# Performance work log

Hardware: AMD Instinct MI355X
Metric: run time of the kernel (lower is better)

The kernel has to match this reference:

```python
import jax, jax.numpy as jnp
import numpy as np

N, D, H, F = 384, 512, 8, 64  # n_nodes, in/out features, heads, per-head hidden
SLOPE = 0.2


def gat_v2_layer(x, mask, W_l, W_r, a):
    """GATv2 layer (is_concat=True). x: [N, D_in]; mask: [N, N, 1] bool.

    torch semantics: g_sum[i, j] = g_l[j] + g_r[i]; e = a . LeakyReLU(g_sum);
    softmax over j (dim=1); aggregate g_r with einsum('ijh,jhf->ihf').
    attn linear nn.Linear(F, 1) is shared across heads -> a: [F].
    """
    n = x.shape[0]
    g_l = (x @ W_l).reshape(n, H, F)
    g_r = (x @ W_r).reshape(n, H, F)
    # pairwise [i, j, h, f] = g_r[i] + g_l[j]  (the big O(N^2) intermediate)
    s = jax.nn.leaky_relu(g_r[:, None] + g_l[None, :], negative_slope=SLOPE)
    e = jnp.einsum('ijhf,f->ijh', s, a)
    e = jnp.where(mask, e, -jnp.inf)
    att = jax.nn.softmax(e, axis=1)  # normalize over source nodes j
    out = jnp.einsum('ijh,jhf->ihf', att, g_r)
    return out.reshape(n, H * F)


def setup_inputs() -> dict:
    key = jax.random.key(0)
    ks = jax.random.split(key, 8)
    x = jax.random.normal(ks[0], (N, D), dtype=jnp.float32)
    adj = jax.random.randint(ks[1], (N, N, 1), 0, 2, dtype=jnp.int32)
    sd = 1.0 / np.sqrt(D)
    sa = 1.0 / np.sqrt(F)
    W_l0 = jax.random.normal(ks[2], (D, H * F), dtype=jnp.float32) * sd
    W_r0 = jax.random.normal(ks[3], (D, H * F), dtype=jnp.float32) * sd
    a0 = jax.random.normal(ks[4], (F,), dtype=jnp.float32) * sa
    W_l1 = jax.random.normal(ks[5], (H * F, H * F), dtype=jnp.float32) * sd
    W_r1 = jax.random.normal(ks[6], (H * F, H * F), dtype=jnp.float32) * sd
    a1 = jax.random.normal(ks[7], (F,), dtype=jnp.float32) * sa
    return {"x": x, "adj": adj, "W_l0": W_l0, "W_r0": W_r0, "a0": a0,
            "W_l1": W_l1, "W_r1": W_r1, "a1": a1}


def reference(x, adj, W_l0, W_r0, a0, W_l1, W_r1, a1):
    n = x.shape[0]
    # selfloop: fill diagonal of adj with 1
    idx = jnp.arange(n)
    adj = adj.at[idx, idx, 0].set(1)
    mask = adj != 0  # [N, N, 1]
    # layer 0: GATv2 -> ELU (i < n_layers-1) -> residual
    out = jax.nn.elu(gat_v2_layer(x, mask, W_l0, W_r0, a0))
    x = x + out
    # layer 1: GATv2 -> Identity -> residual
    out = gat_v2_layer(x, mask, W_l1, W_r1, a1)
    x = x + out
    return x
```

## Files before the change

### kernel.cpp

```cpp
#include <hip/hip_runtime.h>
#include <hip/hip_bf16.h>
#include <stdint.h>

typedef unsigned short ushort_t;
typedef unsigned long long u64;
typedef __attribute__((ext_vector_type(8))) short short8;
typedef __attribute__((ext_vector_type(4))) float f32x4;

#define N_NODES 384
#define HF      512

__device__ inline ushort_t f2bf(float f) {
  __hip_bfloat16 b = __float2bfloat16(f);
  return *reinterpret_cast<ushort_t*>(&b);
}
__device__ inline float bf2f_u(ushort_t u) {
  union { float f; uint32_t i; } v; v.i = ((uint32_t)u) << 16; return v.f;
}

__global__ __launch_bounds__(256) void prep(
    const float* __restrict__ x, const int* __restrict__ adj,
    const float* __restrict__ w0, const float* __restrict__ w1,
    const float* __restrict__ w2, const float* __restrict__ w3,
    ushort_t* __restrict__ WT0, ushort_t* __restrict__ WT1,
    ushort_t* __restrict__ xb, u64* __restrict__ mbits)
{
  const int z = blockIdx.z;
  const int t = threadIdx.x;
  if (z == 4) {
    int idx = (blockIdx.y * 16 + blockIdx.x) * 256 + t;
#pragma unroll
    for (int r = 0; r < 3; ++r) {
      int i = idx + r * 65536;
      xb[i] = f2bf(x[i]);
    }
    return;
  }
  if (z == 5) {
    int b = blockIdx.y * 16 + blockIdx.x;
    if (b >= 96) return;
    int wave = t >> 6, lane = t & 63;
    int row = b * 4 + wave;
#pragma unroll
    for (int w = 0; w < 6; ++w) {
      int j = w * 64 + lane;
      int v = adj[row * N_NODES + j];
      u64 m = __ballot(v != 0 || row == j);
      if (lane == 0) mbits[row * 6 + w] = m;
    }
    return;
  }
  __shared__ ushort_t tile[32][33];
  const float* W = (z == 0) ? w0 : (z == 1) ? w1 : (z == 2) ? w2 : w3;
  ushort_t* WT = ((z < 2) ? WT0 : WT1) + (z & 1) * (512 * 512);
  const int n0 = blockIdx.x * 32, k0 = blockIdx.y * 32;
#pragma unroll
  for (int qq = 0; qq < 4; ++qq) {
    int idx = t + qq * 256, r = idx >> 5, c = idx & 31;
    tile[r][c] = f2bf(W[(k0 + r) * 512 + n0 + c]);
  }
  __syncthreads();
#pragma unroll
  for (int qq = 0; qq < 4; ++qq) {
    int idx = t + qq * 256, r = idx >> 5, c = idx & 31;
    WT[(n0 + r) * 512 + k0 + c] = tile[c][r];
  }
}

__global__ __launch_bounds__(256) void gemm_mfma(
    const ushort_t* __restrict__ A, const ushort_t* __restrict__ WT,
    float* __restrict__ G, ushort_t* __restrict__ glb,
    ushort_t* __restrict__ grT)
{
  const int t = threadIdx.x;
  const int wave = t >> 6, lane = t & 63;
  const int lm = lane & 15, q = lane >> 4;
  const int m0 = blockIdx.x * 16;
  const int n0 = (blockIdx.y * 4 + wave) * 32;

  const short8* Ap = (const short8*)A;
  const short8* Bp = (const short8*)WT;
  const int arow  = (m0 + lm) * 64 + q;
  const int brow0 = (n0 + lm) * 64 + q;
  const int brow1 = (n0 + 16 + lm) * 64 + q;

  f32x4 acc0 = {0.f, 0.f, 0.f, 0.f};
  f32x4 acc1 = {0.f, 0.f, 0.f, 0.f};
#pragma unroll
  for (int kc = 0; kc < 16; ++kc) {
    short8 af = Ap[arow  + kc * 4];
    short8 b0 = Bp[brow0 + kc * 4];
    short8 b1 = Bp[brow1 + kc * 4];
    acc0 = __builtin_amdgcn_mfma_f32_16x16x32_bf16(af, b0, acc0, 0, 0, 0);
    acc1 = __builtin_amdgcn_mfma_f32_16x16x32_bf16(af, b1, acc1, 0, 0, 0);
  }
  if (n0 < 512) {
#pragma unroll
    for (int r = 0; r < 4; ++r) {
      int m = m0 + q * 4 + r;
      glb[m * HF + n0 + lm]      = f2bf(acc0[r]);
      glb[m * HF + n0 + 16 + lm] = f2bf(acc1[r]);
    }
  } else {
#pragma unroll
    for (int r = 0; r < 4; ++r) {
      int m = m0 + q * 4 + r;
      G[m * 1024 + n0 + lm]      = acc0[r];
      G[m * 1024 + n0 + 16 + lm] = acc1[r];
    }
    int c0 = n0 - 512;
    uint2 p0, p1;
    p0.x = (uint32_t)f2bf(acc0[0]) | ((uint32_t)f2bf(acc0[1]) << 16);
    p0.y = (uint32_t)f2bf(acc0[2]) | ((uint32_t)f2bf(acc0[3]) << 16);
    p1.x = (uint32_t)f2bf(acc1[0]) | ((uint32_t)f2bf(acc1[1]) << 16);
    p1.y = (uint32_t)f2bf(acc1[2]) | ((uint32_t)f2bf(acc1[3]) << 16);
    *(uint2*)&grT[(c0 + lm) * 384 + m0 + q * 4]      = p0;
    *(uint2*)&grT[(c0 + 16 + lm) * 384 + m0 + q * 4] = p1;
  }
}

template <int LAYER>
__global__ __launch_bounds__(384) void attn_fused(
    const float* __restrict__ G, const ushort_t* __restrict__ glb,
    const ushort_t* __restrict__ grT, const u64* __restrict__ mbits,
    const float* __restrict__ resid_in, const float* __restrict__ avec,
    float* __restrict__ xcur_out, ushort_t* __restrict__ x1b_out,
    float* __restrict__ f_out)
{
  __shared__ __align__(16) char smem[55296];
  ushort_t (*s_gl)[72]      = (ushort_t(*)[72])smem;
  float    (*s_e)[N_NODES]  = (float(*)[N_NODES])smem;
  ushort_t (*s_pb)[392]     = (ushort_t(*)[392])(smem + 24576);
  __shared__ float s_bri[16];
  __shared__ u64   s_mask[16][6];

  const int t = threadIdx.x;
  const int i0 = blockIdx.x * 16, h = blockIdx.y;
  const int lane = t & 63, wave = t >> 6;

  if (t >= 64 && t < 160) ((u64*)s_mask)[t - 64] = mbits[i0 * 6 + (t - 64)];
  if (t >= 128) {
    int u = t - 128, il = u >> 4, fg = u & 15;
    float4 g4 = *(const float4*)(G + (i0 + il) * 1024 + 512 + h * 64 + fg * 4);
    float4 a4 = *(const float4*)(avec + fg * 4);
    float s = a4.x * g4.x + a4.y * g4.y + a4.z * g4.z + a4.w * g4.w;
    s += __shfl_xor(s, 1); s += __shfl_xor(s, 2);
    s += __shfl_xor(s, 4); s += __shfl_xor(s, 8);
    if (fg == 0) s_bri[il] = s;
  }
#pragma unroll
  for (int rep = 0; rep < 8; ++rep) {
    int idx = rep * 384 + t, row = idx >> 3, c = idx & 7;
    *(short8*)&s_gl[row][c * 8] =
        *(const short8*)&glb[row * HF + h * 64 + c * 8];
  }
  __syncthreads();

  float gl[64];
  {
    const short8* rowp = (const short8*)&s_gl[t][0];
#pragma unroll
    for (int c = 0; c < 8; ++c) {
      short8 v = rowp[c];
#pragma unroll
      for (int u2 = 0; u2 < 8; ++u2)
        gl[c * 8 + u2] = bf2f_u((ushort_t)v[u2]);
    }
  }
  __syncthreads();

  float accl = 0.f;
#pragma unroll
  for (int f = 0; f < 64; ++f) accl += avec[f] * gl[f];

  float e_abs[16];
  for (int il = 0; il < 16; ++il) {
    const float* __restrict__ gr = G + (i0 + il) * 1024 + 512 + h * 64;
    float acc = 0.f;
#pragma unroll
    for (int f = 0; f < 64; ++f) {
      float z = gl[f] + gr[f];
      acc += avec[f] * fabsf(z);
    }
    e_abs[il] = acc;
  }
  {
    const int jw = t >> 6, jb = t & 63;
#pragma unroll
    for (int il = 0; il < 16; ++il) {
      bool m = (s_mask[il][jw] >> jb) & 1;
      float e = 0.6f * (accl + s_bri[il]) + 0.4f * e_abs[il];
      s_e[il][t] = m ? e : -1e30f;
    }
  }
  __syncthreads();

  for (int il = wave; il < 16; il += 6) {
    float v[6];
    float mx = -1e30f;
#pragma unroll
    for (int c = 0; c < 6; ++c) { v[c] = s_e[il][lane + 64 * c]; mx = fmaxf(mx, v[c]); }
#pragma unroll
    for (int off = 32; off; off >>= 1) mx = fmaxf(mx, __shfl_xor(mx, off));
    float sum = 0.f;
#pragma unroll
    for (int c = 0; c < 6; ++c) { v[c] = __expf(v[c] - mx); sum += v[c]; }
#pragma unroll
    for (int off = 32; off; off >>= 1) sum += __shfl_xor(sum, off);
    float inv = 1.0f / sum;
#pragma unroll
    for (int c = 0; c < 6; ++c) s_pb[il][lane + 64 * c] = f2bf(v[c] * inv);
  }
  __syncthreads();

  if (t < 256) {
    const int lm = lane & 15, q = lane >> 4;
    const int f0 = wave * 16;
    const ushort_t* Brow = grT + (h * 64 + f0 + lm) * 384;
    f32x4 acc = {0.f, 0.f, 0.f, 0.f};
#pragma unroll
    for (int kc = 0; kc < 12; ++kc) {
      short8 af = *(const short8*)&s_pb[lm][kc * 32 + q * 8];
      short8 bf = *(const short8*)&Brow[kc * 32 + q * 8];
      acc = __builtin_amdgcn_mfma_f32_16x16x32_bf16(af, bf, acc, 0, 0, 0);
    }
#pragma unroll
    for (int r = 0; r < 4; ++r) {
      int i = i0 + q * 4 + r;
      int off = i * HF + h * 64 + f0 + lm;
      float o = acc[r];
      if (LAYER == 0) {
        float oe = (o > 0.f) ? o : (__expf(o) - 1.f);
        float vv = resid_in[off] + oe;
        xcur_out[off] = vv;
        x1b_out[off]  = f2bf(vv);
      } else {
        f_out[off] = resid_in[off] + o;
      }
    }
  }
}

extern "C" void kernel_launch(void* const* d_in, const int* in_sizes, int n_in,
                              void* d_out, int out_size, void* d_ws, size_t ws_size,
                              hipStream_t stream) {
  const float* x   = (const float*)d_in[0];
  const int*   adj = (const int*)d_in[1];
  const float* Wl0 = (const float*)d_in[2];
  const float* Wr0 = (const float*)d_in[3];
  const float* a0  = (const float*)d_in[4];
  const float* Wl1 = (const float*)d_in[5];
  const float* Wr1 = (const float*)d_in[6];
  const float* a1  = (const float*)d_in[7];
  float* out = (float*)d_out;

  char* ws = (char*)d_ws;
  ushort_t* WT0  = (ushort_t*)(ws + 0L);
  ushort_t* WT1  = (ushort_t*)(ws + (1L << 20));
  ushort_t* xb   = (ushort_t*)(ws + (2L << 20));
  float*    G    = (float*)   (ws + (3L << 20));
  ushort_t* grT  = (ushort_t*)(ws + (5L << 20));
  ushort_t* x1b  = (ushort_t*)(ws + (6L << 20));
  ushort_t* glb  = (ushort_t*)(ws + (7L << 20));
  u64*      mbits= (u64*)     (ws + (8L << 20));
  float*    xcur = (float*)   (ws + (9L << 20));

  prep<<<dim3(16, 16, 6), 256, 0, stream>>>(x, adj, Wl0, Wr0, Wl1, Wr1,
                                            WT0, WT1, xb, mbits);
  gemm_mfma<<<dim3(24, 8), 256, 0, stream>>>(xb, WT0, G, glb, grT);
  attn_fused<0><<<dim3(24, 8), 384, 0, stream>>>(G, glb, grT, mbits, x, a0,
                                                 xcur, x1b, nullptr);
  gemm_mfma<<<dim3(24, 8), 256, 0, stream>>>(x1b, WT1, G, glb, grT);
  attn_fused<1><<<dim3(24, 8), 384, 0, stream>>>(G, glb, grT, mbits, xcur, a1,
                                                 nullptr, nullptr, out);
}
```

Baseline: 137.0 us.

## Halve attention row tile to 8 rows, doubling blocks, and vectorize score loop

The attention kernel now handles 8 destination rows per block instead of 16, so the grid grows from 24x8 to 48x8 blocks and fills more CUs on the GPU. The attention vector is held in registers, gr is read as float4, and the mask and score write are fused into the per-row loop, which removes the e_abs array. Because the MFMA tile is still 16 rows, the unused half of the probability tile is zero-padded and its output rows are skipped. In exchange, each block wastes half of its MFMA work and every block must reload the 384x64 g_l slice for its head, which doubles those loads.

```diff
diff --git a/kernel.cpp b/kernel.cpp
--- a/kernel.cpp
+++ b/kernel.cpp
@@ -130,16 +130,16 @@
   __shared__ __align__(16) char smem[55296];
   ushort_t (*s_gl)[72]      = (ushort_t(*)[72])smem;
   float    (*s_e)[N_NODES]  = (float(*)[N_NODES])smem;
-  ushort_t (*s_pb)[392]     = (ushort_t(*)[392])(smem + 24576);
-  __shared__ float s_bri[16];
-  __shared__ u64   s_mask[16][6];
+  ushort_t (*s_pb)[392]     = (ushort_t(*)[392])(smem + 12288);
+  __shared__ float s_bri[8];
+  __shared__ u64   s_mask[8][6];
 
   const int t = threadIdx.x;
-  const int i0 = blockIdx.x * 16, h = blockIdx.y;
+  const int i0 = blockIdx.x * 8, h = blockIdx.y;
   const int lane = t & 63, wave = t >> 6;
 
-  if (t >= 64 && t < 160) ((u64*)s_mask)[t - 64] = mbits[i0 * 6 + (t - 64)];
-  if (t >= 128) {
+  if (t >= 256 && t < 304) ((u64*)s_mask)[t - 256] = mbits[i0 * 6 + (t - 256)];
+  if (t >= 128 && t < 256) {
     int u = t - 128, il = u >> 4, fg = u & 15;
     float4 g4 = *(const float4*)(G + (i0 + il) * 1024 + 512 + h * 64 + fg * 4);
     float4 a4 = *(const float4*)(avec + fg * 4);
@@ -156,7 +156,7 @@
   }
   __syncthreads();
 
-  float gl[64];
+  float gl[64], av[64];
   {
     const short8* rowp = (const short8*)&s_gl[t][0];
 #pragma unroll
@@ -166,36 +166,43 @@
       for (int u2 = 0; u2 < 8; ++u2)
         gl[c * 8 + u2] = bf2f_u((ushort_t)v[u2]);
     }
-  }
-  __syncthreads();
-
+#pragma unroll
+    for (int c = 0; c < 16; ++c) {
+      float4 a4 = ((const float4*)avec)[c];
+      av[c * 4] = a4.x; av[c * 4 + 1] = a4.y;
+      av[c * 4 + 2] = a4.z; av[c * 4 + 3] = a4.w;
+    }
+  }
   float accl = 0.f;
 #pragma unroll
-  for (int f = 0; f < 64; ++f) accl += avec[f] * gl[f];
-
-  float e_abs[16];
-  for (int il = 0; il < 16; ++il) {
-    const float* __restrict__ gr = G + (i0 + il) * 1024 + 512 + h * 64;
+  for (int f = 0; f < 64; ++f) accl += av[f] * gl[f];
+  __syncthreads();
+
+  const int jw = t >> 6, jb = t & 63;
+#pragma unroll
+  for (int il = 0; il < 8; ++il) {
+    const float4* gr4 = (const float4*)(G + (i0 + il) * 1024 + 512 + h * 64);
     float acc = 0.f;
 #pragma unroll
-    for (int f = 0; f < 64; ++f) {
-      float z = gl[f] + gr[f];
-      acc += avec[f] * fabsf(z);
-    }
-    e_abs[il] = acc;
+    for (int c = 0; c < 16; ++c) {
+      float4 g4 = gr4[c];
+      acc += av[c * 4]     * fabsf(gl[c * 4]     + g4.x);
+      acc += av[c * 4 + 1] * fabsf(gl[c * 4 + 1] + g4.y);
+      acc += av[c * 4 + 2] * fabsf(gl[c * 4 + 2] + g4.z);
+      acc += av[c * 4 + 3] * fabsf(gl[c * 4 + 3] + g4.w);
+    }
+    bool m = (s_mask[il][jw] >> jb) & 1;
+    float e = 0.6f * (accl + s_bri[il]) + 0.4f * acc;
+    s_e[il][t] = m ? e : -1e30f;
   }
   {
-    const int jw = t >> 6, jb = t & 63;
-#pragma unroll
-    for (int il = 0; il < 16; ++il) {
-      bool m = (s_mask[il][jw] >> jb) & 1;
-      float e = 0.6f * (accl + s_bri[il]) + 0.4f * e_abs[il];
-      s_e[il][t] = m ? e : -1e30f;
-    }
-  }
-  __syncthreads();
-
-  for (int il = wave; il < 16; il += 6) {
+    ushort_t z0 = 0;
+#pragma unroll
+    for (int r8 = 0; r8 < 8; ++r8) s_pb[8 + r8][t] = z0;
+  }
+  __syncthreads();
+
+  for (int il = wave; il < 8; il += 6) {
     float v[6];
     float mx = -1e30f;
 #pragma unroll
@@ -224,18 +231,20 @@
       short8 bf = *(const short8*)&Brow[kc * 32 + q * 8];
       acc = __builtin_amdgcn_mfma_f32_16x16x32_bf16(af, bf, acc, 0, 0, 0);
     }
-#pragma unroll
-    for (int r = 0; r < 4; ++r) {
-      int i = i0 + q * 4 + r;
-      int off = i * HF + h * 64 + f0 + lm;
-      float o = acc[r];
-      if (LAYER == 0) {
-        float oe = (o > 0.f) ? o : (__expf(o) - 1.f);
-        float vv = resid_in[off] + oe;
-        xcur_out[off] = vv;
-        x1b_out[off]  = f2bf(vv);
-      } else {
-        f_out[off] = resid_in[off] + o;
+    if (q < 2) {
+#pragma unroll
+      for (int r = 0; r < 4; ++r) {
+        int i = i0 + q * 4 + r;
+        int off = i * HF + h * 64 + f0 + lm;
+        float o = acc[r];
+        if (LAYER == 0) {
+          float oe = (o > 0.f) ? o : (__expf(o) - 1.f);
+          float vv = resid_in[off] + oe;
+          xcur_out[off] = vv;
+          x1b_out[off]  = f2bf(vv);
+        } else {
+          f_out[off] = resid_in[off] + o;
+        }
       }
     }
   }
@@ -268,9 +277,9 @@
   prep<<<dim3(16, 16, 6), 256, 0, stream>>>(x, adj, Wl0, Wr0, Wl1, Wr1,
                                             WT0, WT1, xb, mbits);
   gemm_mfma<<<dim3(24, 8), 256, 0, stream>>>(xb, WT0, G, glb, grT);
-  attn_fused<0><<<dim3(24, 8), 384, 0, stream>>>(G, glb, grT, mbits, x, a0,
+  attn_fused<0><<<dim3(48, 8), 384, 0, stream>>>(G, glb, grT, mbits, x, a0,
                                                  xcur, x1b, nullptr);
   gemm_mfma<<<dim3(24, 8), 256, 0, stream>>>(x1b, WT1, G, glb, grT);
-  attn_fused<1><<<dim3(24, 8), 384, 0, stream>>>(G, glb, grT, mbits, xcur, a1,
+  attn_fused<1><<<dim3(48, 8), 384, 0, stream>>>(G, glb, grT, mbits, xcur, a1,
                                                  nullptr, nullptr, out);
 }
```

Result: faster. 131.5 us (-4.0%).
